# Optimization experiments

Hardware: AMD Instinct MI355X
Metric: run time of the kernel (lower is better)

The kernel has to match this reference:

```python
import jax, jax.numpy as jnp
import numpy as np

B, F, C, W_, H_ = 4, 8, 256, 7, 7   # batch, frames, compressed channels (in_dim//r), width, height
CIN = 2048                          # in_dim
CH = CIN // 16                      # in_dim // (2*r) = 128, per-branch q/k channels


def _pw2d(x, W, b):
    # 1x1 Conv2d == per-pixel channel matmul. x: (N,Cin,H,W), W: (Cout,Cin)
    return jnp.einsum('nchw,oc->nohw', x, W) + b[None, :, None, None]


def setup_inputs() -> dict:
    key = jax.random.key(0)
    ks = iter(jax.random.split(key, 40))
    def rn(shape, s=0.02):
        return jax.random.normal(next(ks), shape, dtype=jnp.float32) * s
    inp = {
        'x':       rn((B * F, CIN, H_, W_), 1.0),
        'domainX': rn((B * F, CIN, H_, W_), 1.0),
        'domainY': rn((B * F, 1, H_, W_), 1.0),
        # conv1_1_pre (1 -> 2048), output is discarded in forward but computed faithfully
        'w_pre': rn((CIN, 1)), 'b_pre': rn((CIN,)),
        # conv3 (2048 -> 256); its weight is SHARED with layer1_downconv and layer1_downconv_Y
        'w_conv3': rn((C, CIN)), 'b_conv3': rn((C,)),
        # value_conv 1x1x1 Conv3d (256 -> 2048); weight SHARED with layer1_upconv(_Y)
        'w_value': rn((CIN, C)), 'b_value': rn((CIN,)),
        # tied-weight convs have their own biases
        'b_l1down': rn((C,)), 'b_l1up': rn((CIN,)),
        'b_l1down_Y': rn((C,)), 'b_l1up_Y': rn((CIN,)),
        # layer2 convs: independent weights (layer2_*gamma init to 0, so init add is a no-op)
        'w_l2down': rn((C, CIN)), 'b_l2down': rn((C,)),
        'w_l2up': rn((CIN, C)), 'b_l2up': rn((CIN,)),
        'w_l2down_Y': rn((C, CIN)), 'b_l2down_Y': rn((C,)),
        'w_l2up_Y': rn((CIN, C)), 'b_l2up_Y': rn((CIN,)),
        # q/k projections (2048 -> 128 each)
        'w_c11': rn((CH, CIN)), 'b_c11': rn((CH,)),
        'w_c12': rn((CH, CIN)), 'b_c12': rn((CH,)),
        'w_c21': rn((CH, CIN)), 'b_c21': rn((CH,)),
        'w_c22': rn((CH, CIN)), 'b_c22': rn((CH,)),
        'pos_embedV': rn((1, F, C * H_ * W_), 1.0),
        'gamma': jnp.asarray(0.01, dtype=jnp.float32),
    }
    return inp


def reference(x, domainX, domainY, w_pre, b_pre, w_conv3, b_conv3, w_value, b_value,
              b_l1down, b_l1up, b_l1down_Y, b_l1up_Y,
              w_l2down, b_l2down, w_l2up, b_l2up,
              w_l2down_Y, b_l2down_Y, w_l2up_Y, b_l2up_Y,
              w_c11, b_c11, w_c12, b_c12, w_c21, b_c21, w_c22, b_c22,
              pos_embedV, gamma):
    S = F * W_ * H_  # 392 tokens per clip
    # conv1_1_pre output is overwritten in the original forward (dead computation)
    _dead = _pw2d(domainY, w_pre, b_pre)
    del _dead
    # domainY path: down(conv3 weight) -> up(value_conv weight) -> layer2 down -> layer2 up
    # (create5D/create4D + permutes + 1x1x1 conv3d collapse to pointwise channel matmuls)
    dY = _pw2d(_pw2d(_pw2d(_pw2d(domainX, w_conv3, b_l1down_Y), w_value, b_l1up_Y),
                     w_l2down_Y, b_l2down_Y), w_l2up_Y, b_l2up_Y)
    q4 = jnp.concatenate([_pw2d(x, w_c11, b_c11), _pw2d(dY, w_c12, b_c12)], axis=1)  # (32,256,7,7)
    q = q4.reshape(B, F, C, W_, H_).transpose(0, 1, 3, 4, 2).reshape(B, S, C)
    # domainX path (same structure, shared layer1 weights, its own biases)
    dX = _pw2d(_pw2d(_pw2d(_pw2d(domainX, w_conv3, b_l1down), w_value, b_l1up),
                     w_l2down, b_l2down), w_l2up, b_l2up)
    k4 = jnp.concatenate([_pw2d(x, w_c21, b_c21), _pw2d(dX, w_c22, b_c22)], axis=1)
    k5 = k4.reshape(B, F, C, W_, H_).transpose(0, 1, 3, 4, 2)        # (B,F,W,H,C)
    k = k5.transpose(0, 2, 1, 3, 4).reshape(B, C, S)                 # faithful odd permute
    # value: conv3 -> +pos_embed -> rearrange to (B, S, C)
    v4 = _pw2d(x, w_conv3, b_conv3)                                  # (32,256,7,7)
    v = v4.reshape(B, F, C * W_ * H_) + pos_embedV                   # dropout p=0 is identity
    v = v.reshape(B, F, C, W_, H_).transpose(0, 1, 3, 4, 2).reshape(B, S, C)
    attn = jax.nn.softmax(jnp.einsum('bnc,bcm->bnm', q, k), axis=-1)  # (B,392,392)
    out = jnp.einsum('bnm,bmc->bnc', attn, v)
    out = out.reshape(B, F, W_, H_, C).transpose(0, 4, 1, 2, 3)      # (B,C,F,W,H)
    out = jnp.einsum('bcthw,oc->bothw', out, w_value) + b_value[None, :, None, None, None]
    out = out.transpose(0, 2, 1, 3, 4).reshape(B * F, CIN, W_, H_)
    return (gamma * out + x) * out + x
```

## Files before the change

kernel.cpp:

```cpp
#include <hip/hip_runtime.h>
#include <hip/hip_bf16.h>


typedef __attribute__((ext_vector_type(8))) short short8;
typedef __attribute__((ext_vector_type(4))) float f32x4;

#define TOKENS 1568

__device__ __forceinline__ ushort f2bf(float f) {
    uint32_t u = __float_as_uint(f);
    u += 0x7fffu + ((u >> 16) & 1u);
    return (ushort)(u >> 16);
}
__device__ __forceinline__ float bf2f(ushort h) { return __uint_as_float(((uint32_t)h) << 16); }
__device__ __forceinline__ void split2(float v, ushort& h, ushort& l) {
    h = f2bf(v); l = f2bf(v - bf2f(h));
}

__device__ __forceinline__ void gl16(const void* g, void* l) {
    __builtin_amdgcn_global_load_lds(
        (const __attribute__((address_space(1))) unsigned int*)g,
        (__attribute__((address_space(3))) unsigned int*)l, 16, 0, 0);
}

#define EPI_PART  0
#define EPI_BF16  1
#define EPI_SPLIT 2
#define EPI_FINAL 3

template<int EPI, int SPL>
__global__ __launch_bounds__(256)
void gmm(const ushort* __restrict__ Ah, const ushort* __restrict__ Al, int lda, long sA,
         const ushort* __restrict__ Wh, const ushort* __restrict__ Wl, int ldw, long sW,
         const float* __restrict__ bias, int sB,
         int nkc, int Kc,
         float* __restrict__ fO, ushort* __restrict__ bO, ushort* __restrict__ bO2,
         int ldc, long sC, int M, int N,
         const float* __restrict__ ex, const float* __restrict__ gamma,
         float* __restrict__ fout)
{
    constexpr bool HASL = (SPL >= 1);
    __shared__ __align__(16) ushort sA_h[2][64 * 32];
    __shared__ __align__(16) ushort sW_h[2][128 * 32];
    __shared__ __align__(16) ushort sA_l[HASL ? 2 : 1][HASL ? 64 * 32 : 8];
    __shared__ __align__(16) ushort sW_l[HASL ? 2 : 1][HASL ? 128 * 32 : 8];

    const int tid = threadIdx.x;
    const int bz = blockIdx.z / nkc;
    const int kc = blockIdx.z % nkc;
    const int row0 = blockIdx.y * 64, col0 = blockIdx.x * 128;
    const bool sp = (SPL == 1) || (SPL == 2 && blockIdx.x < 2);

    const int srow = tid >> 2;
    const int sq   = (tid & 3) ^ (srow & 3);
    int am  = row0 + srow;      if (am  > M - 1) am  = M - 1;
    int wn0 = col0 + srow;      if (wn0 > N - 1) wn0 = N - 1;
    int wn1 = col0 + 64 + srow; if (wn1 > N - 1) wn1 = N - 1;
    const long kbase = (long)kc * Kc + sq * 8;
    const ushort* gA  = Ah + bz * sA + (long)am  * lda + kbase;
    const ushort* gW0 = Wh + bz * sW + (long)wn0 * ldw + kbase;
    const ushort* gW1 = Wh + bz * sW + (long)wn1 * ldw + kbase;
    const ushort *gAl = nullptr, *gWl0 = nullptr, *gWl1 = nullptr;
    if constexpr (HASL) {
        if (sp) {
            gAl  = Al + bz * sA + (long)am  * lda + kbase;
            gWl0 = Wl + bz * sW + (long)wn0 * ldw + kbase;
            gWl1 = Wl + bz * sW + (long)wn1 * ldw + kbase;
        }
    }
    const int wb = (tid & 192) * 8;

    auto STAGE = [&](int buf, int k0) {
        gl16(gA + k0, &sA_h[buf][wb]);
        gl16(gW0 + k0, &sW_h[buf][wb]);
        gl16(gW1 + k0, &sW_h[buf][2048 + wb]);
        if constexpr (HASL) {
            if (sp) {
                gl16(gAl + k0, &sA_l[buf][wb]);
                gl16(gWl0 + k0, &sW_l[buf][wb]);
                gl16(gWl1 + k0, &sW_l[buf][2048 + wb]);
            }
        }
    };

    const int lane = tid & 63, wv = tid >> 6;
    const int wr = (wv >> 1) * 32, wc = (wv & 1) * 64;
    const int fr = lane & 15;
    const int ksw = ((lane >> 4) ^ (lane & 3)) * 8;
    int aoff[2], boff[4];
#pragma unroll
    for (int mi = 0; mi < 2; ++mi) aoff[mi] = (wr + mi * 16 + fr) * 32 + ksw;
#pragma unroll
    for (int ni = 0; ni < 4; ++ni) boff[ni] = (wc + ni * 16 + fr) * 32 + ksw;

    f32x4 acc[2][4];
#pragma unroll
    for (int mi = 0; mi < 2; ++mi)
#pragma unroll
        for (int ni = 0; ni < 4; ++ni) acc[mi][ni] = (f32x4){0.f, 0.f, 0.f, 0.f};

    STAGE(0, 0);
    __syncthreads();
    int cur = 0;
    for (int k0 = 0; k0 < Kc; k0 += 32) {
        if (k0 + 32 < Kc) STAGE(cur ^ 1, k0 + 32);

        short8 fa[2], fb[4];
#pragma unroll
        for (int mi = 0; mi < 2; ++mi) fa[mi] = *(const short8*)&sA_h[cur][aoff[mi]];
#pragma unroll
        for (int ni = 0; ni < 4; ++ni) fb[ni] = *(const short8*)&sW_h[cur][boff[ni]];
#pragma unroll
        for (int mi = 0; mi < 2; ++mi)
#pragma unroll
            for (int ni = 0; ni < 4; ++ni)
                acc[mi][ni] = __builtin_amdgcn_mfma_f32_16x16x32_bf16(fa[mi], fb[ni], acc[mi][ni], 0, 0, 0);
        if constexpr (HASL) {
            if (sp) {
                short8 ga[2], gb[4];
#pragma unroll
                for (int mi = 0; mi < 2; ++mi) ga[mi] = *(const short8*)&sA_l[cur][aoff[mi]];
#pragma unroll
                for (int ni = 0; ni < 4; ++ni) gb[ni] = *(const short8*)&sW_l[cur][boff[ni]];
#pragma unroll
                for (int mi = 0; mi < 2; ++mi)
#pragma unroll
                    for (int ni = 0; ni < 4; ++ni) {
                        acc[mi][ni] = __builtin_amdgcn_mfma_f32_16x16x32_bf16(fa[mi], gb[ni], acc[mi][ni], 0, 0, 0);
                        acc[mi][ni] = __builtin_amdgcn_mfma_f32_16x16x32_bf16(ga[mi], fb[ni], acc[mi][ni], 0, 0, 0);
                    }
            }
        }
        __syncthreads();
        cur ^= 1;
    }

    const int q4 = (lane >> 4) * 4;
    float g = 0.f;
    if constexpr (EPI == EPI_FINAL) g = gamma[0];
#pragma unroll
    for (int mi = 0; mi < 2; ++mi)
#pragma unroll
        for (int ni = 0; ni < 4; ++ni)
#pragma unroll
            for (int qi = 0; qi < 4; ++qi) {
                int m = row0 + wr + mi * 16 + q4 + qi;
                int n = col0 + wc + ni * 16 + fr;
                if (m >= M || n >= N) continue;
                float v = acc[mi][ni][qi];
                if (bias) v += bias[bz * sB + n];
                if constexpr (EPI == EPI_PART) {
                    fO[(long)blockIdx.z * sC + (long)m * ldc + n] = v;
                } else if constexpr (EPI == EPI_BF16) {
                    bO[(long)blockIdx.z * sC + (long)m * ldc + n] = f2bf(v);
                } else if constexpr (EPI == EPI_SPLIT) {
                    long o = (long)blockIdx.z * sC + (long)m * ldc + n;
                    ushort h, l; split2(v, h, l);
                    bO[o] = h; bO2[o] = l;
                } else {
                    int nimg = m / 49, p = m % 49;
                    long xi = (long)nimg * (2048 * 49) + (long)n * 49 + p;
                    float xv = ex[xi];
                    fout[xi] = (g * v + xv) * v + xv;
                }
            }
}

__global__ __launch_bounds__(256)
void prep(const float* c11, const float* c21, const float* conv3,
          const float* c22, const float* c12, const float* wval,
          const float* b_c11, const float* b_c21, const float* b_conv3,
          const float* x, const float* dX,
          ushort* Wg1h, ushort* Wg1l, ushort* C2h, ushort* C2l, ushort* Wvalb,
          float* bg1,
          ushort* Xth, ushort* Xtl, ushort* DXth, ushort* DXtl)
{
    __shared__ float tile[64][65];
    int b = blockIdx.x;
    int tid = threadIdx.x;
    if (b < 8194) {
        int e = b * 256 + tid;
        if (e < 1048576) {
            float v = e < 262144 ? c11[e] : e < 524288 ? c21[e - 262144] : conv3[e - 524288];
            ushort h, l; split2(v, h, l); Wg1h[e] = h; Wg1l[e] = l;
        } else if (e < 1572864) {
            int i = e - 1048576;
            float v = i < 262144 ? c22[i] : c12[i - 262144];
            ushort h, l; split2(v, h, l); C2h[i] = h; C2l[i] = l;
        } else if (e < 2097152) {
            int i = e - 1572864; Wvalb[i] = f2bf(wval[i]);
        } else if (e < 2097664) {
            int i = e - 2097152;
            bg1[i] = i < 128 ? b_c11[i] : i < 256 ? b_c21[i - 128] : b_conv3[i - 256];
        }
    } else {
        int local = b - 8194;
        int z = local >> 10;
        int rem = local & 1023;
        int n = rem & 31, c0 = (rem >> 5) * 64;
        const float* src = z ? dX : x;
        ushort* oh = z ? DXth : Xth;
        ushort* ol = z ? DXtl : Xtl;
        const float* s = src + (long)n * (2048 * 49) + (long)c0 * 49;
        for (int idx = tid; idx < 64 * 49; idx += 256)
            tile[idx / 49][idx % 49] = s[idx];
        __syncthreads();
        for (int idx = tid; idx < 49 * 64; idx += 256) {
            int p = idx >> 6, cl = idx & 63;
            float v = tile[cl][p];
            long o = (long)(n * 49 + p) * 2048 + c0 + cl;
            ushort h, l; split2(v, h, l);
            oh[o] = h; ol[o] = l;
        }
    }
}

__global__ __launch_bounds__(256)
void wtrans(const float* w2u, const float* w2uY, const float* w2d, const float* w2dY,
            const float* wv, const float* w3,
            ushort* W2uTh, ushort* W2uTl, ushort* W2dTh, ushort* W2dTl,
            ushort* WvTh, ushort* WvTl, ushort* W3Th, ushort* W3Tl)
{
    __shared__ float tile[64][65];
    int z = blockIdx.y;
    const float* src; ushort *dh, *dl; int rows;
    switch (z) {
        case 0:  src = w2u;  dh = W2uTh;          dl = W2uTl;          rows = 2048; break;
        case 1:  src = w2uY; dh = W2uTh + 524288; dl = W2uTl + 524288; rows = 2048; break;
        case 2:  src = w2d;  dh = W2dTh;          dl = W2dTl;          rows = 256;  break;
        case 3:  src = w2dY; dh = W2dTh + 524288; dl = W2dTl + 524288; rows = 256;  break;
        case 4:  src = wv;   dh = WvTh;           dl = WvTl;           rows = 2048; break;
        default: src = w3;   dh = W3Th;           dl = W3Tl;           rows = 256;  break;
    }
    int cols = 524288 / rows;
    int tilesX = cols >> 6;
    int t = blockIdx.x;
    int tx = t % tilesX, ty = t / tilesX;
    for (int i = threadIdx.x; i < 4096; i += 256) {
        int r = i >> 6, c = i & 63;
        tile[r][c] = src[(long)(ty * 64 + r) * cols + tx * 64 + c];
    }
    __syncthreads();
    for (int i = threadIdx.x; i < 4096; i += 256) {
        int c = i >> 6, r = i & 63;
        float v = tile[r][c];
        ushort h, l; split2(v, h, l);
        long o = (long)(tx * 64 + c) * rows + ty * 64 + r;
        dh[o] = h; dl[o] = l;
    }
}

__global__ __launch_bounds__(256)
void r_g1(const float* __restrict__ P, const float* __restrict__ bg1,
          const float* __restrict__ pos,
          ushort* Qh, ushort* Ql, ushort* KmH, ushort* KmL, ushort* Vh)
{
    int idx = blockIdx.x * 256 + threadIdx.x;
    int m = idx >> 9, n = idx & 511;
    float v = P[idx] + P[802816 + idx] + P[1605632 + idx] + P[2408448 + idx] + bg1[n];
    int p = m % 49, img = m / 49;
    int f = img & 7, b = img >> 3;
    if (n < 128) {
        ushort h, l; split2(v, h, l);
        Qh[m * 256 + n] = h; Ql[m * 256 + n] = l;
    } else if (n < 256) {
        int c = n - 128;
        int flat = (p / 7) * 14336 + f * 1792 + (p % 7) * 256 + c;
        int ci = flat / 392, mm = flat % 392;
        long o = (long)b * 100352 + (long)mm * 256 + ci;
        ushort h, l; split2(v, h, l);
        KmH[o] = h; KmL[o] = l;
    } else {
        int c = n - 256;
        v += pos[f * 12544 + c * 49 + p];
        int s = m % 392;
        long o = (long)b * 106496 + (long)c * 416 + s;
        Vh[o] = f2bf(v);
        if (s < 24) Vh[o + 392] = 0;
    }
}

__global__ __launch_bounds__(256)
void r_qk2(const float* __restrict__ P, const float* __restrict__ kc,
           ushort* Qh, ushort* Ql, ushort* KmH, ushort* KmL)
{
    int idx = blockIdx.x * 256 + threadIdx.x;
    int m = idx >> 8, j = idx & 255;
    float v = P[idx] + P[401408 + idx] + P[802816 + idx] + P[1204224 + idx] + kc[j];
    ushort h, l; split2(v, h, l);
    if (j < 128) {
        int c = 128 + j;
        int p = m % 49, img = m / 49, f = img & 7, b = img >> 3;
        int flat = (p / 7) * 14336 + f * 1792 + (p % 7) * 256 + c;
        int ci = flat / 392, mm = flat % 392;
        long o = (long)b * 100352 + (long)mm * 256 + ci;
        KmH[o] = h; KmL[o] = l;
    } else {
        Qh[m * 256 + j] = h; Ql[m * 256 + j] = l;
    }
}

__global__ __launch_bounds__(256)
void r_s(const float* __restrict__ P, ushort* __restrict__ Oh, ushort* __restrict__ Ol,
         const ushort* __restrict__ A1h, const ushort* __restrict__ A1l,
         const ushort* __restrict__ A2h, const ushort* __restrict__ A2l,
         const float* __restrict__ c22, const float* __restrict__ c12,
         const float* __restrict__ b1dX, const float* __restrict__ b1uX,
         const float* __restrict__ b2dX, const float* __restrict__ b2uX,
         const float* __restrict__ b1dY, const float* __restrict__ b1uY,
         const float* __restrict__ b2dY, const float* __restrict__ b2uY,
         const float* __restrict__ bc22, const float* __restrict__ bc12,
         float* __restrict__ kc)
{
    int tid = threadIdx.x;
    int blk = blockIdx.x;
    int idx = blk * 256 + tid;
    int br = idx >> 15, e = idx & 32767;
    const float* p = P + (long)br * 524288;
    float v = 0.f;
#pragma unroll
    for (int k = 0; k < 16; ++k) v += p[k * 32768 + e];
    ushort h, l; split2(v, h, l);
    Oh[idx] = h; Ol[idx] = l;

    if (kc) {
        int z = blk >> 7, i = blk & 127;
        const float* b1d = z ? b1dY : b1dX;
        const float* b1u = z ? b1uY : b1uX;
        const float* b2d = z ? b2dY : b2dX;
        const float* b2u = z ? b2uY : b2uX;
        const float* cw  = (z ? c12 : c22) + (long)i * 2048;
        const ushort* a1h = A1h + (long)blk * 256;
        const ushort* a1l = A1l + (long)blk * 256;
        const ushort* a2h = A2h + (long)blk * 2048;
        const ushort* a2l = A2l + (long)blk * 2048;
        float acc = v * b1d[tid];
        acc = fmaf(bf2f(a1h[tid]) + bf2f(a1l[tid]), b2d[tid], acc);
#pragma unroll
        for (int u = 0; u < 8; ++u) {
            int c = u * 256 + tid;
            acc = fmaf(bf2f(a2h[c]) + bf2f(a2l[c]), b1u[c], acc);
            acc = fmaf(cw[c], b2u[c], acc);
        }
        __shared__ float red[4];
        for (int off = 32; off; off >>= 1) acc += __shfl_down(acc, off, 64);
        if ((tid & 63) == 0) red[tid >> 6] = acc;
        __syncthreads();
        if (tid == 0)
            kc[blk] = red[0] + red[1] + red[2] + red[3] + (z ? bc12 : bc22)[i];
    }
}

__global__ __launch_bounds__(256)
void softmax_bf16(const float* __restrict__ P, ushort* __restrict__ attn)
{
    int row = blockIdx.x * 4 + (threadIdx.x >> 6);
    int lane = threadIdx.x & 63;
    int b = row / 392, mm = row % 392;
    const float* r0 = P + (long)(b * 2) * 163072 + (long)mm * 416;
    const float* r1 = r0 + 163072;
    ushort* op = attn + (long)row * 416;
    float v[7]; float mx = -1e30f;
#pragma unroll
    for (int i = 0; i < 7; ++i) {
        int c = lane + i * 64;
        v[i] = (c < 392) ? (r0[c] + r1[c]) : -1e30f;
        mx = fmaxf(mx, v[i]);
    }
    for (int off = 32; off; off >>= 1) mx = fmaxf(mx, __shfl_xor(mx, off, 64));
    float s = 0.f;
#pragma unroll
    for (int i = 0; i < 7; ++i) { v[i] = __expf(v[i] - mx); s += v[i]; }
    for (int off = 32; off; off >>= 1) s += __shfl_xor(s, off, 64);
    float inv = 1.f / s;
#pragma unroll
    for (int i = 0; i < 7; ++i) {
        int c = lane + i * 64;
        if (c < 392) op[c] = f2bf(v[i] * inv);
        else if (c < 416) op[c] = 0;
    }
}

extern "C" void kernel_launch(void* const* d_in, const int* in_sizes, int n_in,
                              void* d_out, int out_size, void* d_ws, size_t ws_size,
                              hipStream_t stream)
{
    const float* x        = (const float*)d_in[0];
    const float* domainX  = (const float*)d_in[1];
    const float* w_conv3  = (const float*)d_in[5];
    const float* b_conv3  = (const float*)d_in[6];
    const float* w_value  = (const float*)d_in[7];
    const float* b_value  = (const float*)d_in[8];
    const float* b_l1down   = (const float*)d_in[9];
    const float* b_l1up     = (const float*)d_in[10];
    const float* b_l1down_Y = (const float*)d_in[11];
    const float* b_l1up_Y   = (const float*)d_in[12];
    const float* w_l2down   = (const float*)d_in[13];
    const float* b_l2down   = (const float*)d_in[14];
    const float* w_l2up     = (const float*)d_in[15];
    const float* b_l2up     = (const float*)d_in[16];
    const float* w_l2down_Y = (const float*)d_in[17];
    const float* b_l2down_Y = (const float*)d_in[18];
    const float* w_l2up_Y   = (const float*)d_in[19];
    const float* b_l2up_Y   = (const float*)d_in[20];
    const float* w_c11 = (const float*)d_in[21];
    const float* b_c11 = (const float*)d_in[22];
    const float* w_c12 = (const float*)d_in[23];
    const float* b_c12 = (const float*)d_in[24];
    const float* w_c21 = (const float*)d_in[25];
    const float* b_c21 = (const float*)d_in[26];
    const float* w_c22 = (const float*)d_in[27];
    const float* b_c22 = (const float*)d_in[28];
    const float* pos   = (const float*)d_in[29];
    const float* gamma = (const float*)d_in[30];
    float* out = (float*)d_out;

    ushort* U = (ushort*)d_ws;
    float*  Fp = (float*)d_ws;

    const long oXt_h   = 0;
    const long oXt_l   = 3211264;
    const long oDXt_h  = 6422528;
    const long oDXt_l  = 9633792;
    const long oWg1_h  = 12845056;
    const long oWg1_l  = 13893632;
    const long oWval   = 14942208;
    const long fPG1    = 7733248;
    const long oC2_h   = 21889024;
    const long oC2_l   = 22413312;
    const long oQ_h    = 0;
    const long oQ_l    = 401408;
    const long oKm_h   = 802816;
    const long oKm_l   = 1204224;
    const long oVT     = 1605632;
    const long oW2uT_h = 2031616;
    const long oW2uT_l = 3080192;
    const long oW2dT_h = 4128768;
    const long oW2dT_l = 5177344;
    const long oWvT_h  = 12845056;
    const long oWvT_l  = 13369344;
    const long oW3T_h  = 13893632;
    const long oW3T_l  = 14417920;
    const long fSpart  = 7733248;
    const long oA1_h   = 17563648;
    const long oA1_l   = 17629184;
    const long oA2_h   = 17694720;
    const long oA2_l   = 18219008;
    const long oA3_h   = 18743296;
    const long oA3_l   = 18808832;
    const long oM_h    = 18874368;
    const long oM_l    = 19398656;
    const long fPG2    = 9961472;
    const long fPL     = 3211264;
    const long oattn   = 9031680;
    const long oO      = 9683968;
    const long fbg1    = 11600000;
    const long fkc     = 11600512;

    prep<<<dim3(10242), 256, 0, stream>>>(
        w_c11, w_c21, w_conv3, w_c22, w_c12, w_value,
        b_c11, b_c21, b_conv3, x, domainX,
        U + oWg1_h, U + oWg1_l, U + oC2_h, U + oC2_l, U + oWval, Fp + fbg1,
        U + oXt_h, U + oXt_l, U + oDXt_h, U + oDXt_l);
    gmm<EPI_PART, 2><<<dim3(4, 25, 4), 256, 0, stream>>>(
        U + oXt_h, U + oXt_l, 2048, 0, U + oWg1_h, U + oWg1_l, 2048, 0,
        nullptr, 0, 4, 512, Fp + fPG1, nullptr, nullptr, 512, 802816L, TOKENS, 512,
        nullptr, nullptr, nullptr);
    r_g1<<<dim3(3136), 256, 0, stream>>>(Fp + fPG1, Fp + fbg1, pos,
        U + oQ_h, U + oQ_l, U + oKm_h, U + oKm_l, U + oVT);
    wtrans<<<dim3(128, 6), 256, 0, stream>>>(w_l2up, w_l2up_Y, w_l2down, w_l2down_Y,
                                             w_value, w_conv3,
                                             U + oW2uT_h, U + oW2uT_l,
                                             U + oW2dT_h, U + oW2dT_l,
                                             U + oWvT_h, U + oWvT_l,
                                             U + oW3T_h, U + oW3T_l);
    gmm<EPI_PART, 1><<<dim3(2, 2, 32), 256, 0, stream>>>(
        U + oC2_h, U + oC2_l, 2048, 262144, U + oW2uT_h, U + oW2uT_l, 2048, 524288,
        nullptr, 0, 16, 128, Fp + fSpart, nullptr, nullptr, 256, 32768L, 128, 256,
        nullptr, nullptr, nullptr);
    r_s<<<dim3(256), 256, 0, stream>>>(Fp + fSpart, U + oA1_h, U + oA1_l,
        nullptr, nullptr, nullptr, nullptr, nullptr, nullptr,
        nullptr, nullptr, nullptr, nullptr, nullptr, nullptr, nullptr, nullptr,
        nullptr, nullptr, nullptr);
    gmm<EPI_SPLIT, 1><<<dim3(16, 2, 2), 256, 0, stream>>>(
        U + oA1_h, U + oA1_l, 256, 32768, U + oW2dT_h, U + oW2dT_l, 256, 524288,
        nullptr, 0, 1, 256, nullptr, U + oA2_h, U + oA2_l, 2048, 262144L, 128, 2048,
        nullptr, nullptr, nullptr);
    gmm<EPI_PART, 1><<<dim3(2, 2, 32), 256, 0, stream>>>(
        U + oA2_h, U + oA2_l, 2048, 262144, U + oWvT_h, U + oWvT_l, 2048, 0,
        nullptr, 0, 16, 128, Fp + fSpart, nullptr, nullptr, 256, 32768L, 128, 256,
        nullptr, nullptr, nullptr);
    r_s<<<dim3(256), 256, 0, stream>>>(Fp + fSpart, U + oA3_h, U + oA3_l,
        U + oA1_h, U + oA1_l, U + oA2_h, U + oA2_l, w_c22, w_c12,
        b_l1down, b_l1up, b_l2down, b_l2up,
        b_l1down_Y, b_l1up_Y, b_l2down_Y, b_l2up_Y,
        b_c22, b_c12, Fp + fkc);
    gmm<EPI_SPLIT, 1><<<dim3(16, 2, 2), 256, 0, stream>>>(
        U + oA3_h, U + oA3_l, 256, 32768, U + oW3T_h, U + oW3T_l, 256, 0,
        nullptr, 0, 1, 256, nullptr, U + oM_h, U + oM_l, 2048, 262144L, 128, 2048,
        nullptr, nullptr, nullptr);
    gmm<EPI_PART, 1><<<dim3(2, 25, 4), 256, 0, stream>>>(
        U + oDXt_h, U + oDXt_l, 2048, 0, U + oM_h, U + oM_l, 2048, 0,
        nullptr, 0, 4, 512, Fp + fPG2, nullptr, nullptr, 256, 401408L, TOKENS, 256,
        nullptr, nullptr, nullptr);
    r_qk2<<<dim3(1568), 256, 0, stream>>>(Fp + fPG2, Fp + fkc,
        U + oQ_h, U + oQ_l, U + oKm_h, U + oKm_l);
    gmm<EPI_PART, 1><<<dim3(4, 7, 8), 256, 0, stream>>>(
        U + oQ_h, U + oQ_l, 256, 100352, U + oKm_h, U + oKm_l, 256, 100352,
        nullptr, 0, 2, 128, Fp + fPL, nullptr, nullptr, 416, 163072L, 392, 392,
        nullptr, nullptr, nullptr);
    softmax_bf16<<<dim3(392), 256, 0, stream>>>(Fp + fPL, U + oattn);
    gmm<EPI_BF16, 0><<<dim3(2, 7, 4), 256, 0, stream>>>(
        U + oattn, nullptr, 416, 163072, U + oVT, nullptr, 416, 106496,
        nullptr, 0, 1, 416, nullptr, U + oO, nullptr, 256, 100352L, 392, 256,
        nullptr, nullptr, nullptr);
    gmm<EPI_FINAL, 0><<<dim3(16, 25, 1), 256, 0, stream>>>(
        U + oO, nullptr, 256, 0, U + oWval, nullptr, 256, 0,
        b_value, 0, 1, 256, nullptr, nullptr, nullptr, 0, 0L, TOKENS, 2048,
        x, gamma, out);
}
```

Measured before the change: 173.8 us.

## Fuse attention QK, softmax and PV into one kernel; merge weight transpose with reduction

Replaces the three-launch attention path (split-K QK^T GEMM writing fp32 partials, a softmax kernel, and a PV GEMM) with one fused kernel. Each wave computes 16 query rows against all 392 keys in registers, applies softmax, stages the bf16 probabilities in LDS and multiplies by V directly. This removes the fp32 logits and attention-matrix round trips through global memory and two launches. It also merges the weight transpose kernel into the r_g1 reduction kernel as extra blocks, saving one more launch. The trade-off is that the fused attention grid is only 28 blocks, so it uses far fewer CUs and holds many registers per thread.

```diff
diff --git a/kernel.cpp b/kernel.cpp
--- a/kernel.cpp
+++ b/kernel.cpp
@@ -216,67 +216,68 @@
 }
 
 __global__ __launch_bounds__(256)
-void wtrans(const float* w2u, const float* w2uY, const float* w2d, const float* w2dY,
+void rg1_wt(const float* __restrict__ P, const float* __restrict__ bg1,
+            const float* __restrict__ pos,
+            ushort* Qh, ushort* Ql, ushort* KmH, ushort* KmL, ushort* Vh,
+            const float* w2u, const float* w2uY, const float* w2d, const float* w2dY,
             const float* wv, const float* w3,
             ushort* W2uTh, ushort* W2uTl, ushort* W2dTh, ushort* W2dTl,
             ushort* WvTh, ushort* WvTl, ushort* W3Th, ushort* W3Tl)
 {
     __shared__ float tile[64][65];
-    int z = blockIdx.y;
-    const float* src; ushort *dh, *dl; int rows;
-    switch (z) {
-        case 0:  src = w2u;  dh = W2uTh;          dl = W2uTl;          rows = 2048; break;
-        case 1:  src = w2uY; dh = W2uTh + 524288; dl = W2uTl + 524288; rows = 2048; break;
-        case 2:  src = w2d;  dh = W2dTh;          dl = W2dTl;          rows = 256;  break;
-        case 3:  src = w2dY; dh = W2dTh + 524288; dl = W2dTl + 524288; rows = 256;  break;
-        case 4:  src = wv;   dh = WvTh;           dl = WvTl;           rows = 2048; break;
-        default: src = w3;   dh = W3Th;           dl = W3Tl;           rows = 256;  break;
-    }
-    int cols = 524288 / rows;
-    int tilesX = cols >> 6;
-    int t = blockIdx.x;
-    int tx = t % tilesX, ty = t / tilesX;
-    for (int i = threadIdx.x; i < 4096; i += 256) {
-        int r = i >> 6, c = i & 63;
-        tile[r][c] = src[(long)(ty * 64 + r) * cols + tx * 64 + c];
-    }
-    __syncthreads();
-    for (int i = threadIdx.x; i < 4096; i += 256) {
-        int c = i >> 6, r = i & 63;
-        float v = tile[r][c];
-        ushort h, l; split2(v, h, l);
-        long o = (long)(tx * 64 + c) * rows + ty * 64 + r;
-        dh[o] = h; dl[o] = l;
-    }
-}
-
-__global__ __launch_bounds__(256)
-void r_g1(const float* __restrict__ P, const float* __restrict__ bg1,
-          const float* __restrict__ pos,
-          ushort* Qh, ushort* Ql, ushort* KmH, ushort* KmL, ushort* Vh)
-{
-    int idx = blockIdx.x * 256 + threadIdx.x;
-    int m = idx >> 9, n = idx & 511;
-    float v = P[idx] + P[802816 + idx] + P[1605632 + idx] + P[2408448 + idx] + bg1[n];
-    int p = m % 49, img = m / 49;
-    int f = img & 7, b = img >> 3;
-    if (n < 128) {
-        ushort h, l; split2(v, h, l);
-        Qh[m * 256 + n] = h; Ql[m * 256 + n] = l;
-    } else if (n < 256) {
-        int c = n - 128;
-        int flat = (p / 7) * 14336 + f * 1792 + (p % 7) * 256 + c;
-        int ci = flat / 392, mm = flat % 392;
-        long o = (long)b * 100352 + (long)mm * 256 + ci;
-        ushort h, l; split2(v, h, l);
-        KmH[o] = h; KmL[o] = l;
+    int blk = blockIdx.x;
+    int tid = threadIdx.x;
+    if (blk < 3136) {
+        int idx = blk * 256 + tid;
+        int m = idx >> 9, n = idx & 511;
+        float v = P[idx] + P[802816 + idx] + P[1605632 + idx] + P[2408448 + idx] + bg1[n];
+        int p = m % 49, img = m / 49;
+        int f = img & 7, b = img >> 3;
+        if (n < 128) {
+            ushort h, l; split2(v, h, l);
+            Qh[m * 256 + n] = h; Ql[m * 256 + n] = l;
+        } else if (n < 256) {
+            int c = n - 128;
+            int flat = (p / 7) * 14336 + f * 1792 + (p % 7) * 256 + c;
+            int ci = flat / 392, mm = flat % 392;
+            long o = (long)b * 100352 + (long)mm * 256 + ci;
+            ushort h, l; split2(v, h, l);
+            KmH[o] = h; KmL[o] = l;
+        } else {
+            int c = n - 256;
+            v += pos[f * 12544 + c * 49 + p];
+            int s = m % 392;
+            long o = (long)b * 106496 + (long)c * 416 + s;
+            Vh[o] = f2bf(v);
+            if (s < 24) Vh[o + 392] = 0;
+        }
     } else {
-        int c = n - 256;
-        v += pos[f * 12544 + c * 49 + p];
-        int s = m % 392;
-        long o = (long)b * 106496 + (long)c * 416 + s;
-        Vh[o] = f2bf(v);
-        if (s < 24) Vh[o + 392] = 0;
+        int t6 = blk - 3136;
+        int z = t6 >> 7, t = t6 & 127;
+        const float* src; ushort *dh, *dl; int rows;
+        switch (z) {
+            case 0:  src = w2u;  dh = W2uTh;          dl = W2uTl;          rows = 2048; break;
+            case 1:  src = w2uY; dh = W2uTh + 524288; dl = W2uTl + 524288; rows = 2048; break;
+            case 2:  src = w2d;  dh = W2dTh;          dl = W2dTl;          rows = 256;  break;
+            case 3:  src = w2dY; dh = W2dTh + 524288; dl = W2dTl + 524288; rows = 256;  break;
+            case 4:  src = wv;   dh = WvTh;           dl = WvTl;           rows = 2048; break;
+            default: src = w3;   dh = W3Th;           dl = W3Tl;           rows = 256;  break;
+        }
+        int cols = 524288 / rows;
+        int tilesX = cols >> 6;
+        int tx = t % tilesX, ty = t / tilesX;
+        for (int i = tid; i < 4096; i += 256) {
+            int r = i >> 6, c = i & 63;
+            tile[r][c] = src[(long)(ty * 64 + r) * cols + tx * 64 + c];
+        }
+        __syncthreads();
+        for (int i = tid; i < 4096; i += 256) {
+            int c = i >> 6, r = i & 63;
+            float v = tile[r][c];
+            ushort h, l; split2(v, h, l);
+            long o = (long)(tx * 64 + c) * rows + ty * 64 + r;
+            dh[o] = h; dl[o] = l;
+        }
     }
 }
 
@@ -352,32 +353,95 @@
 }
 
 __global__ __launch_bounds__(256)
-void softmax_bf16(const float* __restrict__ P, ushort* __restrict__ attn)
-{
-    int row = blockIdx.x * 4 + (threadIdx.x >> 6);
-    int lane = threadIdx.x & 63;
-    int b = row / 392, mm = row % 392;
-    const float* r0 = P + (long)(b * 2) * 163072 + (long)mm * 416;
-    const float* r1 = r0 + 163072;
-    ushort* op = attn + (long)row * 416;
-    float v[7]; float mx = -1e30f;
-#pragma unroll
-    for (int i = 0; i < 7; ++i) {
-        int c = lane + i * 64;
-        v[i] = (c < 392) ? (r0[c] + r1[c]) : -1e30f;
-        mx = fmaxf(mx, v[i]);
-    }
-    for (int off = 32; off; off >>= 1) mx = fmaxf(mx, __shfl_xor(mx, off, 64));
-    float s = 0.f;
-#pragma unroll
-    for (int i = 0; i < 7; ++i) { v[i] = __expf(v[i] - mx); s += v[i]; }
-    for (int off = 32; off; off >>= 1) s += __shfl_xor(s, off, 64);
-    float inv = 1.f / s;
-#pragma unroll
-    for (int i = 0; i < 7; ++i) {
-        int c = lane + i * 64;
-        if (c < 392) op[c] = f2bf(v[i] * inv);
-        else if (c < 416) op[c] = 0;
+void fattn(const ushort* __restrict__ Qh, const ushort* __restrict__ Ql,
+           const ushort* __restrict__ Kmh, const ushort* __restrict__ Kml,
+           const ushort* __restrict__ VT, ushort* __restrict__ O)
+{
+    __shared__ ushort Pl[4][16 * 424];
+    const int b = blockIdx.y;
+    const int r0 = blockIdx.x * 64;
+    const int tid = threadIdx.x;
+    const int lane = tid & 63, wv = tid >> 6;
+    const int fr = lane & 15, kb = (lane >> 4) * 8;
+    const int rw = r0 + wv * 16;
+    const long base = (long)b * 100352;
+    const long vbase = (long)b * 106496;
+
+    int qr = rw + fr; if (qr > 391) qr = 391;
+    const ushort* qph = Qh + base + (long)qr * 256 + kb;
+    const ushort* qpl = Ql + base + (long)qr * 256 + kb;
+    short8 qh[8], ql[8];
+#pragma unroll
+    for (int kf = 0; kf < 8; ++kf) {
+        qh[kf] = *(const short8*)(qph + kf * 32);
+        ql[kf] = *(const short8*)(qpl + kf * 32);
+    }
+
+    f32x4 lg[26];
+#pragma unroll
+    for (int nf = 0; nf < 26; ++nf) {
+        int kcol = nf * 16 + fr; if (kcol > 391) kcol = 391;
+        const ushort* kph = Kmh + base + (long)kcol * 256 + kb;
+        const ushort* kpl = Kml + base + (long)kcol * 256 + kb;
+        f32x4 a = (f32x4){0.f, 0.f, 0.f, 0.f};
+#pragma unroll
+        for (int kf = 0; kf < 8; ++kf) {
+            short8 bh = *(const short8*)(kph + kf * 32);
+            short8 bl = *(const short8*)(kpl + kf * 32);
+            a = __builtin_amdgcn_mfma_f32_16x16x32_bf16(qh[kf], bh, a, 0, 0, 0);
+            a = __builtin_amdgcn_mfma_f32_16x16x32_bf16(qh[kf], bl, a, 0, 0, 0);
+            a = __builtin_amdgcn_mfma_f32_16x16x32_bf16(ql[kf], bh, a, 0, 0, 0);
+        }
+        lg[nf] = a;
+    }
+
+    if (fr >= 8) {
+#pragma unroll
+        for (int q = 0; q < 4; ++q) lg[24][q] = -1e30f;
+    }
+#pragma unroll
+    for (int q = 0; q < 4; ++q) lg[25][q] = -1e30f;
+
+    float inv[4];
+#pragma unroll
+    for (int q = 0; q < 4; ++q) {
+        float m = -1e30f;
+#pragma unroll
+        for (int nf = 0; nf < 26; ++nf) m = fmaxf(m, lg[nf][q]);
+        for (int off = 8; off; off >>= 1) m = fmaxf(m, __shfl_xor(m, off, 64));
+        float s = 0.f;
+#pragma unroll
+        for (int nf = 0; nf < 26; ++nf) { float e = __expf(lg[nf][q] - m); lg[nf][q] = e; s += e; }
+        for (int off = 8; off; off >>= 1) s += __shfl_xor(s, off, 64);
+        inv[q] = 1.f / s;
+    }
+
+    ushort* pw = &Pl[wv][0];
+#pragma unroll
+    for (int nf = 0; nf < 26; ++nf)
+#pragma unroll
+        for (int q = 0; q < 4; ++q) {
+            int rr = (lane >> 4) * 4 + q;
+            pw[rr * 424 + nf * 16 + fr] = f2bf(lg[nf][q] * inv[q]);
+        }
+    __syncthreads();
+
+#pragma unroll
+    for (int cf = 0; cf < 16; ++cf) {
+        f32x4 o = (f32x4){0.f, 0.f, 0.f, 0.f};
+        const ushort* vp = VT + vbase + (long)(cf * 16 + fr) * 416 + kb;
+#pragma unroll
+        for (int kf = 0; kf < 13; ++kf) {
+            short8 pa = *(const short8*)&pw[fr * 424 + kf * 32 + kb];
+            short8 vb = *(const short8*)(vp + kf * 32);
+            o = __builtin_amdgcn_mfma_f32_16x16x32_bf16(pa, vb, o, 0, 0, 0);
+        }
+#pragma unroll
+        for (int q = 0; q < 4; ++q) {
+            int orow = rw + (lane >> 4) * 4 + q;
+            if (orow < 392)
+                O[base + (long)orow * 256 + cf * 16 + fr] = f2bf(o[q]);
+        }
     }
 }
 
@@ -451,8 +515,6 @@
     const long oM_h    = 18874368;
     const long oM_l    = 19398656;
     const long fPG2    = 9961472;
-    const long fPL     = 3211264;
-    const long oattn   = 9031680;
     const long oO      = 9683968;
     const long fbg1    = 11600000;
     const long fkc     = 11600512;
@@ -466,14 +528,11 @@
         U + oXt_h, U + oXt_l, 2048, 0, U + oWg1_h, U + oWg1_l, 2048, 0,
         nullptr, 0, 4, 512, Fp + fPG1, nullptr, nullptr, 512, 802816L, TOKENS, 512,
         nullptr, nullptr, nullptr);
-    r_g1<<<dim3(3136), 256, 0, stream>>>(Fp + fPG1, Fp + fbg1, pos,
-        U + oQ_h, U + oQ_l, U + oKm_h, U + oKm_l, U + oVT);
-    wtrans<<<dim3(128, 6), 256, 0, stream>>>(w_l2up, w_l2up_Y, w_l2down, w_l2down_Y,
-                                             w_value, w_conv3,
-                                             U + oW2uT_h, U + oW2uT_l,
-                                             U + oW2dT_h, U + oW2dT_l,
-                                             U + oWvT_h, U + oWvT_l,
-                                             U + oW3T_h, U + oW3T_l);
+    rg1_wt<<<dim3(3904), 256, 0, stream>>>(Fp + fPG1, Fp + fbg1, pos,
+        U + oQ_h, U + oQ_l, U + oKm_h, U + oKm_l, U + oVT,
+        w_l2up, w_l2up_Y, w_l2down, w_l2down_Y, w_value, w_conv3,
+        U + oW2uT_h, U + oW2uT_l, U + oW2dT_h, U + oW2dT_l,
+        U + oWvT_h, U + oWvT_l, U + oW3T_h, U + oW3T_l);
     gmm<EPI_PART, 1><<<dim3(2, 2, 32), 256, 0, stream>>>(
         U + oC2_h, U + oC2_l, 2048, 262144, U + oW2uT_h, U + oW2uT_l, 2048, 524288,
         nullptr, 0, 16, 128, Fp + fSpart, nullptr, nullptr, 256, 32768L, 128, 256,
@@ -505,15 +564,8 @@
         nullptr, nullptr, nullptr);
     r_qk2<<<dim3(1568), 256, 0, stream>>>(Fp + fPG2, Fp + fkc,
         U + oQ_h, U + oQ_l, U + oKm_h, U + oKm_l);
-    gmm<EPI_PART, 1><<<dim3(4, 7, 8), 256, 0, stream>>>(
-        U + oQ_h, U + oQ_l, 256, 100352, U + oKm_h, U + oKm_l, 256, 100352,
-        nullptr, 0, 2, 128, Fp + fPL, nullptr, nullptr, 416, 163072L, 392, 392,
-        nullptr, nullptr, nullptr);
-    softmax_bf16<<<dim3(392), 256, 0, stream>>>(Fp + fPL, U + oattn);
-    gmm<EPI_BF16, 0><<<dim3(2, 7, 4), 256, 0, stream>>>(
-        U + oattn, nullptr, 416, 163072, U + oVT, nullptr, 416, 106496,
-        nullptr, 0, 1, 416, nullptr, U + oO, nullptr, 256, 100352L, 392, 256,
-        nullptr, nullptr, nullptr);
+    fattn<<<dim3(7, 4), 256, 0, stream>>>(
+        U + oQ_h, U + oQ_l, U + oKm_h, U + oKm_l, U + oVT, U + oO);
     gmm<EPI_FINAL, 0><<<dim3(16, 25, 1), 256, 0, stream>>>(
         U + oO, nullptr, 256, 0, U + oWval, nullptr, 256, 0,
         b_value, 0, 1, 256, nullptr, nullptr, nullptr, 0, 0L, TOKENS, 2048,
```

Measured after the change: 229.8 us. 32.2% more time.
